# Kernel optimization log

Hardware: AMD Instinct MI355X
Metric: run time of the kernel (lower is better)

Reference implementation:

```python
import jax, jax.numpy as jnp
import numpy as np

PI = float(np.pi)


def _conv2d(x, w, b, pad):
    out = jax.lax.conv_general_dilated(x, w, (1, 1), ((pad, pad), (pad, pad)),
                                       dimension_numbers=('NCHW', 'OIHW', 'NCHW'))
    return out + b[None, :, None, None]


def _group_norm(x, gamma, beta, groups, eps=1e-5):
    B, C, h, w = x.shape
    xg = x.reshape(B, groups, C // groups, h, w)
    mu = xg.mean(axis=(2, 3, 4), keepdims=True)
    var = xg.var(axis=(2, 3, 4), keepdims=True)
    xn = ((xg - mu) / jnp.sqrt(var + eps)).reshape(B, C, h, w)
    return xn * gamma[None, :, None, None] + beta[None, :, None, None]


def _l2n(x, eps=1e-12):
    return x / jnp.maximum(jnp.linalg.norm(x, axis=1, keepdims=True), eps)


def _dense_sift(x):
    # kornia DenseSIFTDescriptor defaults: 8 ang bins, 4x4 spatial bins,
    # spatial_bin_size=4, rootsift=True, clipval=0.2, stride=1, padding=1
    eps = 1e-10
    NA = 8
    # 'diff' spatial gradient with replicate padding, normalized (/2)
    xp = jnp.pad(x, ((0, 0), (0, 0), (1, 1), (1, 1)), mode='edge')
    gx = (xp[:, :, 1:-1, 2:] - xp[:, :, 1:-1, :-2]) * 0.5
    gy = (xp[:, :, 2:, 1:-1] - xp[:, :, :-2, 1:-1]) * 0.5
    mag = jnp.sqrt(gx * gx + gy * gy + eps)[:, 0]           # [B,H,W]
    ori = jnp.arctan2(gy, gx + eps)[:, 0] + 2.0 * PI
    o_big = NA * ori / (2.0 * PI)
    bo0f = jnp.floor(o_big)
    wo1_ = o_big - bo0f
    wo0 = (1.0 - wo1_) * mag
    wo1 = wo1_ * mag
    bo0 = bo0f.astype(jnp.int32) % NA
    bo1 = (bo0 + 1) % NA
    bins = jnp.arange(NA).reshape(1, NA, 1, 1)
    ang = ((bo0[:, None] == bins).astype(x.dtype) * wo0[:, None]
           + (bo1[:, None] == bins).astype(x.dtype) * wo1[:, None])  # [B,8,H,W]
    # SIFT pooling kernel ksize=4 (triangle weights), conv pad=2 -> H+1,W+1
    xc2 = np.array([0.5, 1.5, 1.5, 0.5], np.float32)
    pool1 = np.outer(xc2, xc2) / 4.0
    pk = jnp.asarray(np.tile(pool1[None, None], (NA, 1, 1, 1)))  # depthwise [8,1,4,4]
    pooled = jax.lax.conv_general_dilated(ang, pk, (1, 1), ((2, 2), (2, 2)),
                dimension_numbers=('NCHW', 'OIHW', 'NCHW'), feature_group_count=NA)
    # identity reshape conv: 128 = 8 ang * 4*4 spatial bins, pad=1 -> back to H,W
    rk = jnp.asarray(np.eye(128, dtype=np.float32).reshape(128, NA, 4, 4))
    out = jax.lax.conv_general_dilated(pooled, rk, (1, 1), ((1, 1), (1, 1)),
                dimension_numbers=('NCHW', 'OIHW', 'NCHW'))
    out = jnp.clip(_l2n(out), 0.0, 0.2)
    out = _l2n(out)
    l1 = jnp.maximum(jnp.sum(jnp.abs(out), axis=1, keepdims=True), 1e-12)
    return jnp.sqrt(out / l1 + eps)  # rootsift


def _joint_bilateral(x, guide, ksize=5, sigma_color=0.1, sigma_space=1.5):
    pad = ksize // 2
    ax = np.arange(ksize, dtype=np.float32) - ksize // 2
    g1 = np.exp(-ax ** 2 / (2.0 * sigma_space ** 2))
    g1 = g1 / g1.sum()
    sk = np.outer(g1, g1)  # normalized 5x5 gaussian space kernel
    xp = jnp.pad(x, ((0, 0), (0, 0), (pad, pad), (pad, pad)), mode='reflect')
    gp = jnp.pad(guide, ((0, 0), (0, 0), (pad, pad), (pad, pad)), mode='reflect')
    h, w = x.shape[2], x.shape[3]
    inv = -0.5 / (sigma_color ** 2)
    num = jnp.zeros_like(x)
    den = jnp.zeros((x.shape[0], 1, h, w), x.dtype)
    for dy in range(ksize):           # fixed 5x5 tap loop, accumulated in-place
        for dx in range(ksize):
            gs = gp[:, :, dy:dy + h, dx:dx + w]
            cd = jnp.sum(jnp.abs(gs - guide), axis=1, keepdims=True) ** 2  # l1 squared
            wgt = sk[dy, dx] * jnp.exp(inv * cd)
            num = num + wgt * xp[:, :, dy:dy + h, dx:dx + w]
            den = den + wgt
    return num / den


def _forward(x, gt, w1, b1, g1w, g1b, w2, b2, g2w, g2b, w3, b3, g3w, g3b,
             w4, b4, g4w, g4b, w5, b5):
    orig = x
    f = _dense_sift(x)
    f = jax.nn.relu(_group_norm(_conv2d(f, w1, b1, 2), g1w, g1b, 8))
    f = jax.nn.relu(_group_norm(_conv2d(f, w2, b2, 1), g2w, g2b, 8))
    f = jax.nn.relu(_group_norm(_conv2d(f, w3, b3, 1), g3w, g3b, 4))
    f = jax.nn.relu(_group_norm(_conv2d(f, w4, b4, 1), g4w, g4b, 4))
    f = _conv2d(f, w5, b5, 1)
    # rgb_to_yuv(gt)[:, 1:] as guidance
    r, g, b = gt[:, 0], gt[:, 1], gt[:, 2]
    u = -0.147 * r - 0.289 * g + 0.436 * b
    v = 0.615 * r - 0.515 * g - 0.100 * b
    guide = jnp.stack([u, v], axis=1)
    f = _joint_bilateral(f, guide)

    def _rescale(c, lo, hi):
        c = (c - c.min()) / (c.max() - c.min() + 1e-6)  # global min/max over B,H,W
        c = jnp.clip(c, 0.0, 1.0)
        return c * (hi - lo) + lo

    U = _rescale(f[:, 0], -0.436, 0.436)
    V = _rescale(f[:, 1], -0.615, 0.615)
    Y = orig[:, 0]
    R = Y + 1.14 * V
    G = Y - 0.396 * U - 0.581 * V
    B = Y + 2.029 * U
    return jnp.stack([R, G, B], axis=1)


def setup_inputs() -> dict:
    key = jax.random.key(0)
    ks = jax.random.split(key, 16)
    B = 4
    d = {
        'x': jax.random.uniform(ks[0], (B, 1, 270, 512), jnp.float32),
        'gt': jax.random.uniform(ks[1], (B, 3, 270, 512), jnp.float32),
        'w1': jax.random.normal(ks[2], (64, 128, 5, 5), jnp.float32) * 0.02,
        'b1': jnp.zeros((64,), jnp.float32),
        'g1w': jnp.ones((64,), jnp.float32), 'g1b': jnp.zeros((64,), jnp.float32),
        'w2': jax.random.normal(ks[3], (32, 64, 3, 3), jnp.float32) * 0.04,
        'b2': jnp.zeros((32,), jnp.float32),
        'g2w': jnp.ones((32,), jnp.float32), 'g2b': jnp.zeros((32,), jnp.float32),
        'w3': jax.random.normal(ks[4], (16, 32, 3, 3), jnp.float32) * 0.05,
        'b3': jnp.zeros((16,), jnp.float32),
        'g3w': jnp.ones((16,), jnp.float32), 'g3b': jnp.zeros((16,), jnp.float32),
        'w4': jax.random.normal(ks[5], (8, 16, 3, 3), jnp.float32) * 0.08,
        'b4': jnp.zeros((8,), jnp.float32),
        'g4w': jnp.ones((8,), jnp.float32), 'g4b': jnp.zeros((8,), jnp.float32),
        'w5': jax.random.normal(ks[6], (2, 8, 3, 3), jnp.float32) * 0.1,
        'b5': jnp.zeros((2,), jnp.float32),
    }
    return d


def reference(x, gt, w1, b1, g1w, g1b, w2, b2, g2w, g2b, w3, b3, g3w, g3b,
              w4, b4, g4w, g4b, w5, b5):
    return _forward(x, gt, w1, b1, g1w, g1b, w2, b2, g2w, g2b, w3, b3, g3w, g3b,
                    w4, b4, g4w, g4b, w5, b5)
```

## Files before the change

kernel.cpp:

```cpp
#include <hip/hip_runtime.h>

constexpr int NB  = 4;
constexpr int IH  = 270;
constexpr int IW  = 512;
constexpr int NPIX = IH * IW;
constexpr int PH  = 271;
constexpr int PW  = 513;
constexpr float TWO_PI_F = 6.28318530717958647692f;

typedef short  bf16x8 __attribute__((ext_vector_type(8)));
typedef float floatx4 __attribute__((ext_vector_type(4)));

__device__ inline unsigned short f2bf(float x) {
  union { float f; unsigned u; } un; un.f = x;
  unsigned r = un.u + 0x7fff + ((un.u >> 16) & 1);
  return (unsigned short)(r >> 16);
}
__device__ inline float bf2f(unsigned short u) {
  union { unsigned u; float f; } x; x.u = ((unsigned)u) << 16; return x.f;
}
__device__ inline unsigned fkey(float f) {
  unsigned u = __float_as_uint(f);
  return (u & 0x80000000u) ? ~u : (u | 0x80000000u);
}
__device__ inline float funkey(unsigned k) {
  unsigned u = (k & 0x80000000u) ? (k ^ 0x80000000u) : ~k;
  return __uint_as_float(u);
}
__device__ inline void gn_coef_thread(const float* __restrict__ stats,
                                      const float* __restrict__ gamma,
                                      const float* __restrict__ beta,
                                      float* cA, float* cB, int C, int chper, int b) {
  int c = threadIdx.x;
  if (c < C) {
    int g0 = (c / chper) * chper;
    float S = 0.f, S2 = 0.f;
    for (int k = 0; k < chper; k++) {
      S  += stats[(b * C + g0 + k) * 2];
      S2 += stats[(b * C + g0 + k) * 2 + 1];
    }
    double Nd = (double)chper * NPIX;
    double mu = (double)S / Nd;
    double var = (double)S2 / Nd - mu * mu;
    double rstd = 1.0 / sqrt(var + 1e-5);
    float A = (float)rstd * gamma[c];
    cA[c] = A;
    cB[c] = beta[c] - (float)mu * A;
  }
}

__device__ inline void mfma_pack_one(const float* __restrict__ w, short* __restrict__ wB,
                                     int i, int CO, int CI, int KK, int CHUNKS) {
  int j = i & 7, l = (i >> 3) & 63, f = i >> 9;
  int t = f % KK; int fc = f / KK; int cc = fc % CHUNKS; int g = fc / CHUNKS;
  int ci = cc * 32 + ((l >> 4) << 3) + j;
  int co = g * 16 + (l & 15);
  float v = (ci < CI && co < CO) ? w[((size_t)co * CI + ci) * KK + t] : 0.f;
  wB[i] = (short)f2bf(v);
}
__device__ inline void repack_one(const float* __restrict__ w, float* __restrict__ wT,
                                  int i, int CO, int CI, int KK) {
  int o = i / (CI * KK);
  int r = i % (CI * KK);
  int ci = r / KK, kk = r % KK;
  wT[(kk * CI + ci) * CO + o] = w[i];
}
__global__ __launch_bounds__(256) void prep_kernel(
    const float* __restrict__ w1, const float* __restrict__ w2,
    const float* __restrict__ w3, const float* __restrict__ w4,
    const float* __restrict__ w5,
    short* __restrict__ w1B, short* __restrict__ w2B, short* __restrict__ w3B,
    float* __restrict__ w4T, float* __restrict__ w5T) {
  constexpr int N1 = 4 * 4 * 25 * 512;
  constexpr int N2 = 2 * 2 * 9 * 512;
  constexpr int N3 = 1 * 1 * 9 * 512;
  constexpr int N4 = 8 * 16 * 9;
  constexpr int N5 = 2 * 8 * 9;
  int i = blockIdx.x * 256 + threadIdx.x;
  if (i < N1) { mfma_pack_one(w1, w1B, i, 64, 128, 25, 4); return; }
  i -= N1;
  if (i < N2) { mfma_pack_one(w2, w2B, i, 32, 64, 9, 2); return; }
  i -= N2;
  if (i < N3) { mfma_pack_one(w3, w3B, i, 16, 32, 9, 1); return; }
  i -= N3;
  if (i < N4) { repack_one(w4, w4T, i, 8, 16, 9); return; }
  i -= N4;
  if (i < N5) { repack_one(w5, w5T, i, 2, 8, 9); return; }
}

__global__ __launch_bounds__(256) void sift_desc_kernel(
    const float* __restrict__ x, short* __restrict__ descg) {
  const int b = blockIdx.z;
  const int x0 = blockIdx.x * 16, y0 = blockIdx.y * 16;
  __shared__ float xs[24][25];
  __shared__ float wo0[22][23], wo1[22][23];
  __shared__ int   bo0[22][23];
  __shared__ float pooled[8][19][20];
  __shared__ float s1s[256], gs[256];
  const int tid = threadIdx.x;
  const float* xb = x + (size_t)b * NPIX;

  for (int t = tid; t < 576; t += 256) {
    int r = t / 24, c = t % 24;
    int gy = min(max(y0 - 4 + r, 0), IH - 1);
    int gx = min(max(x0 - 4 + c, 0), IW - 1);
    xs[r][c] = xb[gy * IW + gx];
  }
  __syncthreads();

  for (int t = tid; t < 484; t += 256) {
    int r = t / 22, c = t % 22;
    int gy = y0 - 3 + r, gx = x0 - 3 + c;
    float w0 = 0.f, w1v = 0.f; int b0 = 0;
    if (gy >= 0 && gy < IH && gx >= 0 && gx < IW) {
      float gxv = (xs[r + 1][c + 2] - xs[r + 1][c]) * 0.5f;
      float gyv = (xs[r + 2][c + 1] - xs[r][c + 1]) * 0.5f;
      float mag = sqrtf(gxv * gxv + gyv * gyv + 1e-10f);
      float ori = atan2f(gyv, gxv + 1e-10f) + TWO_PI_F;
      float obig = ori * (8.0f / TWO_PI_F);
      float bf = floorf(obig);
      float w1_ = obig - bf;
      w0  = (1.0f - w1_) * mag;
      w1v = w1_ * mag;
      b0  = ((int)bf) & 7;
    }
    wo0[r][c] = w0; wo1[r][c] = w1v; bo0[r][c] = b0;
  }
  __syncthreads();

  const float pwt[4] = {0.25f, 0.75f, 0.75f, 0.25f};
  for (int t = tid; t < 361; t += 256) {
    int pr = t / 19, pc = t % 19;
    int py = y0 - 1 + pr, px = x0 - 1 + pc;
    float acc[8] = {0, 0, 0, 0, 0, 0, 0, 0};
    if (py >= 0 && py < PH && px >= 0 && px < PW) {
      #pragma unroll
      for (int i = 0; i < 4; i++) {
        #pragma unroll
        for (int j = 0; j < 4; j++) {
          float w0 = wo0[pr + i][pc + j], w1v = wo1[pr + i][pc + j];
          int b0 = bo0[pr + i][pc + j];
          int b1i = (b0 + 1) & 7;
          float pw = pwt[i] * pwt[j];
          #pragma unroll
          for (int a = 0; a < 8; a++) {
            float add = (a == b0 ? w0 : 0.f) + (a == b1i ? w1v : 0.f);
            acc[a] = fmaf(pw, add, acc[a]);
          }
        }
      }
    }
    #pragma unroll
    for (int a = 0; a < 8; a++) pooled[a][pr][pc] = acc[a];
  }
  __syncthreads();

  {
    int py = tid >> 4, px = tid & 15;
    int y = y0 + py;
    float s1 = 0.f, g = 0.f;
    if (y < IH) {
      float sum2 = 0.f;
      for (int c = 0; c < 128; c++) {
        int a = c >> 4, i = (c >> 2) & 3, j = c & 3;
        float p = pooled[a][py + i][px + j];
        sum2 = fmaf(p, p, sum2);
      }
      s1 = 1.0f / fmaxf(sqrtf(sum2), 1e-12f);
      float st2 = 0.f, st = 0.f;
      for (int c = 0; c < 128; c++) {
        int a = c >> 4, i = (c >> 2) & 3, j = c & 3;
        float p = pooled[a][py + i][px + j];
        float tv = fminf(p * s1, 0.2f);
        st2 = fmaf(tv, tv, st2);
        st += tv;
      }
      float s2 = 1.0f / fmaxf(sqrtf(st2), 1e-12f);
      float l1 = fmaxf(s2 * st, 1e-12f);
      g = s2 / l1;
    }
    s1s[tid] = s1; gs[tid] = g;
  }
  __syncthreads();

  for (int k = 0; k < 16; k++) {
    int gidx = k * 256 + tid;
    int cc = gidx >> 10, pix = (gidx >> 2) & 255, sub = gidx & 3;
    int py = pix >> 4, px = pix & 15;
    int y = y0 + py;
    if (y >= IH) continue;
    float s1v = s1s[pix], gv = gs[pix];
    int a = cc * 2 + (sub >> 1);
    unsigned short v8[8];
    #pragma unroll
    for (int jj = 0; jj < 8; jj++) {
      int i = (sub * 2 + (jj >> 2)) & 3;
      int j = jj & 3;
      float p = pooled[a][py + i][px + j];
      v8[jj] = f2bf(sqrtf(fminf(p * s1v, 0.2f) * gv + 1e-10f));
    }
    uint4 pk;
    pk.x = (unsigned)v8[0] | ((unsigned)v8[1] << 16);
    pk.y = (unsigned)v8[2] | ((unsigned)v8[3] << 16);
    pk.z = (unsigned)v8[4] | ((unsigned)v8[5] << 16);
    pk.w = (unsigned)v8[6] | ((unsigned)v8[7] << 16);
    size_t base = ((size_t)(b * 4 + cc) * NPIX + (size_t)y * IW + (x0 + px)) * 32 + sub * 8;
    *(uint4*)(descg + base) = pk;
  }
}

__global__ __launch_bounds__(512, 2) void conv1_mfma_kernel(
    const short* __restrict__ descg, const short* __restrict__ w1B,
    const float* __restrict__ bias, unsigned short* __restrict__ out,
    float* __restrict__ stats) {
  const int b = blockIdx.z;
  const int x0 = blockIdx.x * 16, y0 = blockIdx.y * 16;
  __shared__ __align__(16) char smem_raw[33408];
  short* desc = (short*)smem_raw;
  float* cout = (float*)smem_raw;

  const int tid = threadIdx.x;
  const int wave = tid >> 6, lane = tid & 63;
  const int quad = lane >> 4, lm = lane & 15;
  const int nh = wave & 1, mh = wave >> 1;

  floatx4 acc[2][4];
  #pragma unroll
  for (int j = 0; j < 2; j++)
    #pragma unroll
    for (int i = 0; i < 4; i++) acc[j][i] = (floatx4){0.f, 0.f, 0.f, 0.f};

  for (int cc = 0; cc < 4; cc++) {
    __syncthreads();
    const short* dg = descg + (size_t)(b * 4 + cc) * NPIX * 32;
    for (int u = tid; u < 1600; u += 512) {
      int pos = u >> 2, sub = u & 3;
      int r = pos / 20, c = pos % 20;
      int gy = y0 - 2 + r, gx = x0 - 2 + c;
      uint4 val = {0u, 0u, 0u, 0u};
      if (gy >= 0 && gy < IH && gx >= 0 && gx < IW)
        val = *(const uint4*)(dg + ((size_t)gy * IW + gx) * 32 + sub * 8);
      *(uint4*)(desc + pos * 40 + sub * 8) = val;
    }
    __syncthreads();

    const short* wb = w1B + (size_t)cc * 25 * 512 + (lane << 3);
    bf16x8 bfrC[2], bfrN[2];
    #pragma unroll
    for (int j = 0; j < 2; j++)
      bfrN[j] = *(const bf16x8*)(wb + (size_t)(nh * 2 + j) * 100 * 512);
    #pragma unroll
    for (int t = 0; t < 25; t++) {
      int ky = t / 5, kx = t % 5;
      #pragma unroll
      for (int j = 0; j < 2; j++) bfrC[j] = bfrN[j];
      if (t < 24) {
        int t1 = t + 1;
        #pragma unroll
        for (int j = 0; j < 2; j++)
          bfrN[j] = *(const bf16x8*)(wb + ((size_t)(nh * 2 + j) * 100 + t1) * 512);
      }
      bf16x8 av[4];
      #pragma unroll
      for (int i = 0; i < 4; i++)
        av[i] = *(const bf16x8*)(desc + ((mh * 4 + i + ky) * 20 + lm + kx) * 40 + quad * 8);
      #pragma unroll
      for (int j = 0; j < 2; j++)
        #pragma unroll
        for (int i = 0; i < 4; i++)
          acc[j][i] = __builtin_amdgcn_mfma_f32_16x16x32_bf16(av[i], bfrC[j], acc[j][i], 0, 0, 0);
    }
  }

  unsigned short* ob = out + (size_t)b * 64 * NPIX;
  for (int h = 0; h < 2; h++) {
    __syncthreads();
    if (nh == h) {
      #pragma unroll
      for (int j = 0; j < 2; j++)
        #pragma unroll
        for (int i = 0; i < 4; i++)
          #pragma unroll
          for (int r = 0; r < 4; r++)
            cout[(j * 16 + lm) * 261 + (mh * 4 + i) * 16 + quad * 4 + r] = acc[j][i][r];
    }
    __syncthreads();
    for (int v = tid; v < 8192; v += 512) {
      int col = v >> 8, px = v & 255;
      int y = y0 + (px >> 4), x = x0 + (px & 15);
      if (y < IH)
        ob[(size_t)(h * 32 + col) * NPIX + y * IW + x] = f2bf(cout[col * 261 + px] + bias[h * 32 + col]);
    }
    int col = tid >> 4, seg = tid & 15;
    int co = h * 32 + col;
    float bv = bias[co];
    float sum = 0.f, sq = 0.f;
    if (y0 + seg < IH) {
      #pragma unroll
      for (int k = 0; k < 16; k++) {
        float vv = cout[col * 261 + seg * 16 + k] + bv;
        sum += vv; sq += vv * vv;
      }
    }
    sum += __shfl_down(sum, 8, 16); sq += __shfl_down(sq, 8, 16);
    sum += __shfl_down(sum, 4, 16); sq += __shfl_down(sq, 4, 16);
    sum += __shfl_down(sum, 2, 16); sq += __shfl_down(sq, 2, 16);
    sum += __shfl_down(sum, 1, 16); sq += __shfl_down(sq, 1, 16);
    if (seg == 0) {
      atomicAdd(&stats[(b * 64 + co) * 2], sum);
      atomicAdd(&stats[(b * 64 + co) * 2 + 1], sq);
    }
  }
}

template <int CI, int CO, int CHPER, bool STATS>
__global__ __launch_bounds__(256) void convk3_mfma_kernel(
    const unsigned short* __restrict__ xin, const short* __restrict__ wB,
    const float* __restrict__ bias, const float* __restrict__ statsIn,
    const float* __restrict__ gamma, const float* __restrict__ beta,
    float* __restrict__ statsOut, unsigned short* __restrict__ out) {
  constexpr int CHUNKS = CI / 32;
  constexpr int G = CO / 16;
  constexpr int MPW = 2 * G;
  constexpr int CIS = CI + 8;
  constexpr int TILE_B = 180 * CIS * 2;
  constexpr int COUT_B = CO * 133 * 4;
  constexpr int UNION_B = TILE_B > COUT_B ? TILE_B : COUT_B;
  __shared__ __align__(16) char sm[UNION_B + CI * 8];
  short* tile = (short*)sm;
  float* cout = (float*)sm;
  float* cA = (float*)(sm + UNION_B);
  float* cB = cA + CI;

  const int b = blockIdx.z;
  const int x0 = blockIdx.x * 16, y0 = blockIdx.y * 8;
  const int tid = threadIdx.x;
  const int wave = tid >> 6, lane = tid & 63;
  const int quad = lane >> 4, lm = lane & 15;
  const int n = wave % G, mh = wave / G;

  gn_coef_thread(statsIn, gamma, beta, cA, cB, CI, CHPER, b);
  __syncthreads();

  const unsigned short* xb = xin + (size_t)b * CI * NPIX;
  for (int v = tid; v < (CI / 2) * 180; v += 256) {
    int cp = v / 180, pos = v % 180;
    int r = pos / 18, c = pos % 18;
    int gy = y0 - 1 + r, gx = x0 - 1 + c;
    float v0 = 0.f, v1 = 0.f;
    if (gy >= 0 && gy < IH && gx >= 0 && gx < IW) {
      v0 = fmaxf(fmaf(bf2f(xb[(size_t)(2 * cp) * NPIX + gy * IW + gx]), cA[2 * cp], cB[2 * cp]), 0.f);
      v1 = fmaxf(fmaf(bf2f(xb[(size_t)(2 * cp + 1) * NPIX + gy * IW + gx]), cA[2 * cp + 1], cB[2 * cp + 1]), 0.f);
    }
    unsigned pk = (unsigned)f2bf(v0) | ((unsigned)f2bf(v1) << 16);
    *(unsigned*)(tile + pos * CIS + 2 * cp) = pk;
  }
  __syncthreads();

  floatx4 acc[MPW];
  #pragma unroll
  for (int i = 0; i < MPW; i++) acc[i] = (floatx4){0.f, 0.f, 0.f, 0.f};

  constexpr int NT = CHUNKS * 9;
  const short* wbase = wB + ((size_t)n * NT) * 512 + (lane << 3);
  bf16x8 bfrC, avC[MPW], bfrN, avN[MPW];
  bfrN = *(const bf16x8*)(wbase);
  #pragma unroll
  for (int i = 0; i < MPW; i++)
    avN[i] = *(const bf16x8*)(tile + ((mh * MPW + i) * 18 + lm) * CIS + quad * 8);
  #pragma unroll
  for (int t = 0; t < NT; t++) {
    bfrC = bfrN;
    #pragma unroll
    for (int i = 0; i < MPW; i++) avC[i] = avN[i];
    if (t < NT - 1) {
      int t1 = t + 1;
      int cc1 = t1 / 9, r1 = t1 % 9, ky1 = r1 / 3, kx1 = r1 % 3;
      bfrN = *(const bf16x8*)(wbase + (size_t)t1 * 512);
      #pragma unroll
      for (int i = 0; i < MPW; i++)
        avN[i] = *(const bf16x8*)(tile + ((mh * MPW + i + ky1) * 18 + lm + kx1) * CIS + cc1 * 32 + quad * 8);
    }
    #pragma unroll
    for (int i = 0; i < MPW; i++)
      acc[i] = __builtin_amdgcn_mfma_f32_16x16x32_bf16(avC[i], bfrC, acc[i], 0, 0, 0);
  }
  __syncthreads();
  #pragma unroll
  for (int i = 0; i < MPW; i++) {
    #pragma unroll
    for (int r = 0; r < 4; r++) {
      int pixel = (mh * MPW + i) * 16 + quad * 4 + r;
      cout[(n * 16 + lm) * 133 + pixel] = acc[i][r];
    }
  }
  __syncthreads();
  unsigned short* ob = out + (size_t)b * CO * NPIX;
  for (int v = tid; v < CO * 128; v += 256) {
    int co = v >> 7, px = v & 127;
    int y = y0 + (px >> 4), x = x0 + (px & 15);
    if (y < IH) ob[(size_t)co * NPIX + y * IW + x] = f2bf(cout[co * 133 + px] + bias[co]);
  }
  if (STATS) {
    constexpr int TPC = 256 / CO;
    constexpr int PXT = 128 / TPC;
    int col = tid / TPC, seg = tid % TPC;
    float bv = bias[col];
    float sum = 0.f, sq = 0.f;
    #pragma unroll
    for (int k = 0; k < PXT; k++) {
      int p = seg * PXT + k;
      if (y0 + (p >> 4) < IH) {
        float vv = cout[col * 133 + p] + bv;
        sum += vv; sq += vv * vv;
      }
    }
    #pragma unroll
    for (int off = TPC / 2; off > 0; off >>= 1) {
      sum += __shfl_down(sum, off);
      sq  += __shfl_down(sq, off);
    }
    if (seg == 0) {
      atomicAdd(&statsOut[(b * CO + col) * 2], sum);
      atomicAdd(&statsOut[(b * CO + col) * 2 + 1], sq);
    }
  }
}

template <int CI, int CO, int CHPER, bool STATS, bool OUT_BF16>
__global__ __launch_bounds__(256) void convs_kernel(
    const unsigned short* __restrict__ xin, const float* __restrict__ wT,
    const float* __restrict__ bias, const float* __restrict__ statsIn,
    const float* __restrict__ gamma, const float* __restrict__ beta,
    float* __restrict__ statsOut, void* __restrict__ outv) {
  constexpr int OPT = CO / 2;
  const int b = blockIdx.z;
  const int x0 = blockIdx.x * 16, y0 = blockIdx.y * 8;
  __shared__ float tile[CI * 180];
  __shared__ float cA[CI], cB[CI];
  __shared__ float ssum[CO], ssq[CO];
  gn_coef_thread(statsIn, gamma, beta, cA, cB, CI, CHPER, b);
  if (STATS && threadIdx.x < CO) { ssum[threadIdx.x] = 0.f; ssq[threadIdx.x] = 0.f; }
  __syncthreads();
  const unsigned short* xb = xin + (size_t)b * CI * NPIX;
  for (int t = threadIdx.x; t < CI * 180; t += 256) {
    int ci = t / 180, rc = t % 180, r = rc / 18, c = rc % 18;
    int gy = y0 - 1 + r, gx = x0 - 1 + c;
    float v = 0.f;
    if (gy >= 0 && gy < IH && gx >= 0 && gx < IW)
      v = fmaxf(fmaf(bf2f(xb[(size_t)ci * NPIX + gy * IW + gx]), cA[ci], cB[ci]), 0.f);
    tile[t] = v;
  }
  __syncthreads();
  const int t = threadIdx.x;
  const int px = t & 127, og = t >> 7;
  const int pyy = px >> 4, pxx = px & 15;
  const int oc0 = og * OPT;
  const int y = y0 + pyy, x = x0 + pxx;
  float acc[OPT] = {};
  for (int ky = 0; ky < 3; ky++) {
    for (int kx = 0; kx < 3; kx++) {
      const float* wrow = wT + (size_t)((ky * 3 + kx) * CI) * CO + oc0;
      for (int ci = 0; ci < CI; ci++) {
        float v = tile[ci * 180 + (pyy + ky) * 18 + pxx + kx];
        #pragma unroll
        for (int o = 0; o < OPT; o++) acc[o] = fmaf(v, wrow[ci * CO + o], acc[o]);
      }
    }
  }
  if (y < IH) {
    #pragma unroll
    for (int o = 0; o < OPT; o++) {
      float vv = acc[o] + bias[oc0 + o];
      if (OUT_BF16) {
        unsigned short* ob = (unsigned short*)outv + (size_t)b * CO * NPIX;
        ob[(size_t)(oc0 + o) * NPIX + y * IW + x] = f2bf(vv);
      } else {
        float* ob = (float*)outv + (size_t)b * CO * NPIX;
        ob[(size_t)(oc0 + o) * NPIX + y * IW + x] = vv;
      }
      if (STATS) {
        atomicAdd(&ssum[oc0 + o], vv);
        atomicAdd(&ssq[oc0 + o], vv * vv);
      }
    }
  }
  if (STATS) {
    __syncthreads();
    if (threadIdx.x < CO) {
      atomicAdd(&statsOut[(b * CO + threadIdx.x) * 2], ssum[threadIdx.x]);
      atomicAdd(&statsOut[(b * CO + threadIdx.x) * 2 + 1], ssq[threadIdx.x]);
    }
  }
}

__global__ __launch_bounds__(256) void bilateral_kernel(
    const float* __restrict__ f, const float* __restrict__ gt,
    float* __restrict__ out, unsigned* __restrict__ mmbits) {
  const int b = blockIdx.z;
  const int x0 = blockIdx.x * 16, y0 = blockIdx.y * 16;
  __shared__ float gu[20][20], gv[20][20], f0s[20][20], f1s[20][20];
  __shared__ float red[4][4];
  const float* gtb = gt + (size_t)b * 3 * NPIX;
  const float* fb = f + (size_t)b * 2 * NPIX;
  for (int t = threadIdx.x; t < 400; t += 256) {
    int r = t / 20, c = t % 20;
    int gy = y0 - 2 + r, gx = x0 - 2 + c;
    if (gy < 0) gy = -gy;
    if (gy > IH - 1) gy = 2 * (IH - 1) - gy;
    if (gx < 0) gx = -gx;
    if (gx > IW - 1) gx = 2 * (IW - 1) - gx;
    int p = gy * IW + gx;
    float rr = gtb[p], gg = gtb[NPIX + p], bb = gtb[2 * NPIX + p];
    gu[r][c]  = -0.147f * rr - 0.289f * gg + 0.436f * bb;
    gv[r][c]  =  0.615f * rr - 0.515f * gg - 0.100f * bb;
    f0s[r][c] = fb[p];
    f1s[r][c] = fb[NPIX + p];
  }
  __syncthreads();
  const int t = threadIdx.x;
  const int lx = t % 16, ly = t / 16;
  const int y = y0 + ly, x = x0 + lx;
  const bool valid = (y < IH);

  float o0 = 0.f, o1 = 0.f;
  if (valid) {
    float g1v[5];
    float s = 0.f;
    #pragma unroll
    for (int k = 0; k < 5; k++) {
      float a = (float)(k - 2);
      g1v[k] = expf(-a * a / 4.5f);
      s += g1v[k];
    }
    #pragma unroll
    for (int k = 0; k < 5; k++) g1v[k] /= s;
    float cu = gu[ly + 2][lx + 2], cv = gv[ly + 2][lx + 2];
    float num0 = 0.f, num1 = 0.f, den = 0.f;
    #pragma unroll
    for (int dy = 0; dy < 5; dy++) {
      #pragma unroll
      for (int dx = 0; dx < 5; dx++) {
        float du = fabsf(gu[ly + dy][lx + dx] - cu) + fabsf(gv[ly + dy][lx + dx] - cv);
        float wgt = g1v[dy] * g1v[dx] * expf(-50.0f * du * du);
        num0 = fmaf(wgt, f0s[ly + dy][lx + dx], num0);
        num1 = fmaf(wgt, f1s[ly + dy][lx + dx], num1);
        den += wgt;
      }
    }
    o0 = num0 / den; o1 = num1 / den;
    float* ob = out + (size_t)b * 2 * NPIX;
    ob[y * IW + x] = o0;
    ob[NPIX + y * IW + x] = o1;
  }
  float mn0 = valid ? o0 : 1e30f,  mx0 = valid ? o0 : -1e30f;
  float mn1 = valid ? o1 : 1e30f,  mx1 = valid ? o1 : -1e30f;
  #pragma unroll
  for (int off = 32; off > 0; off >>= 1) {
    mn0 = fminf(mn0, __shfl_xor(mn0, off));
    mx0 = fmaxf(mx0, __shfl_xor(mx0, off));
    mn1 = fminf(mn1, __shfl_xor(mn1, off));
    mx1 = fmaxf(mx1, __shfl_xor(mx1, off));
  }
  if ((t & 63) == 0) {
    red[t >> 6][0] = mn0; red[t >> 6][1] = mx0;
    red[t >> 6][2] = mn1; red[t >> 6][3] = mx1;
  }
  __syncthreads();
  if (t == 0) {
    for (int w = 1; w < 4; w++) {
      red[0][0] = fminf(red[0][0], red[w][0]);
      red[0][1] = fmaxf(red[0][1], red[w][1]);
      red[0][2] = fminf(red[0][2], red[w][2]);
      red[0][3] = fmaxf(red[0][3], red[w][3]);
    }
    atomicMax(&mmbits[0], fkey(red[0][1]));
    atomicMax(&mmbits[1], fkey(red[0][3]));
    atomicMin(&mmbits[2], fkey(red[0][0]));
    atomicMin(&mmbits[3], fkey(red[0][2]));
  }
}

__global__ __launch_bounds__(256) void final_kernel(
    const float* __restrict__ bil, const float* __restrict__ x,
    const unsigned* __restrict__ mmbits, float* __restrict__ out) {
  int i = blockIdx.x * 256 + threadIdx.x;
  if (i >= NB * NPIX) return;
  float mx0 = funkey(mmbits[0]), mx1 = funkey(mmbits[1]);
  float mn0 = funkey(mmbits[2]), mn1 = funkey(mmbits[3]);
  int b = i / NPIX, p = i % NPIX;
  float f0 = bil[(size_t)b * 2 * NPIX + p];
  float f1 = bil[(size_t)b * 2 * NPIX + NPIX + p];
  float U = (f0 - mn0) / (mx0 - mn0 + 1e-6f);
  U = fminf(fmaxf(U, 0.f), 1.f) * 0.872f - 0.436f;
  float V = (f1 - mn1) / (mx1 - mn1 + 1e-6f);
  V = fminf(fmaxf(V, 0.f), 1.f) * 1.23f - 0.615f;
  float Y = x[(size_t)b * NPIX + p];
  float* ob = out + (size_t)b * 3 * NPIX;
  ob[p]            = Y + 1.14f * V;
  ob[NPIX + p]     = Y - 0.396f * U - 0.581f * V;
  ob[2 * NPIX + p] = Y + 2.029f * U;
}

extern "C" void kernel_launch(void* const* d_in, const int* in_sizes, int n_in,
                              void* d_out, int out_size, void* d_ws, size_t ws_size,
                              hipStream_t stream) {
  const float* x   = (const float*)d_in[0];
  const float* gt  = (const float*)d_in[1];
  const float* w1  = (const float*)d_in[2];
  const float* b1  = (const float*)d_in[3];
  const float* g1w = (const float*)d_in[4];
  const float* g1b = (const float*)d_in[5];
  const float* w2  = (const float*)d_in[6];
  const float* b2  = (const float*)d_in[7];
  const float* g2w = (const float*)d_in[8];
  const float* g2b = (const float*)d_in[9];
  const float* w3  = (const float*)d_in[10];
  const float* b3  = (const float*)d_in[11];
  const float* g3w = (const float*)d_in[12];
  const float* g3b = (const float*)d_in[13];
  const float* w4  = (const float*)d_in[14];
  const float* b4  = (const float*)d_in[15];
  const float* g4w = (const float*)d_in[16];
  const float* g4b = (const float*)d_in[17];
  const float* w5  = (const float*)d_in[18];
  const float* b5  = (const float*)d_in[19];
  float* out = (float*)d_out;

  char* ws = (char*)d_ws;
  float* stats1 = (float*)ws;
  float* stats2 = stats1 + 512;
  float* stats3 = stats2 + 256;
  float* stats4 = stats3 + 128;
  unsigned* mmbits = (unsigned*)(ws + 12288);
  char* base = ws + 16384;
  short* descg = (short*)base;
  size_t descg_shorts = (size_t)NB * 4 * NPIX * 32;
  unsigned short* bufB_h = (unsigned short*)base;
  float* c5    = (float*)(base + 36000000);
  float* bilat = (float*)(base + 41000000);
  short* w1B = descg + descg_shorts;
  short* w2B = w1B + 204800;
  short* w3B = w2B + 18432;
  float* w4T = (float*)(w3B + 4608);
  float* w5T = w4T + 1152;
  unsigned short* bufA_h = (unsigned short*)(w5T + 144);

  hipMemsetAsync(ws, 0, 12304, stream);
  hipMemsetAsync(ws + 12296, 0xFF, 8, stream);

  prep_kernel<<<896, 256, 0, stream>>>(w1, w2, w3, w4, w5, w1B, w2B, w3B, w4T, w5T);

  sift_desc_kernel<<<dim3(32, 17, NB), 256, 0, stream>>>(x, descg);

  conv1_mfma_kernel<<<dim3(32, 17, NB), 512, 0, stream>>>(descg, w1B, b1, bufA_h, stats1);

  convk3_mfma_kernel<64, 32, 8, true><<<dim3(32, 34, NB), 256, 0, stream>>>(
      bufA_h, w2B, b2, stats1, g1w, g1b, stats2, bufB_h);

  convk3_mfma_kernel<32, 16, 4, true><<<dim3(32, 34, NB), 256, 0, stream>>>(
      bufB_h, w3B, b3, stats2, g2w, g2b, stats3, bufA_h);

  convs_kernel<16, 8, 4, true, true><<<dim3(32, 34, NB), 256, 0, stream>>>(
      bufA_h, w4T, b4, stats3, g3w, g3b, stats4, bufB_h);

  convs_kernel<8, 2, 2, false, false><<<dim3(32, 34, NB), 256, 0, stream>>>(
      bufB_h, w5T, b5, stats4, g4w, g4b, nullptr, c5);

  bilateral_kernel<<<dim3(32, 17, NB), 256, 0, stream>>>(c5, gt, bilat, mmbits);
  final_kernel<<<(NB * NPIX + 255) / 256, 256, 0, stream>>>(bilat, x, mmbits, out);

  (void)in_sizes; (void)n_in; (void)out_size; (void)ws_size;
}
```

Baseline: 1.300 ms.

## Shrink conv1 tiles to 8x8 with 4 waves and reshape weight prefetch

Conv1 now uses 8x8 output tiles with 256-thread blocks, and each wave owns 16 output channels across all 64 pixels. The previous layout used 16x16 tiles, 512 threads and a 2x4 wave split. The smaller tile cuts shared memory and registers, which allows more blocks to be resident. In exchange the halo overhead rises sharply (12x12 loaded per 8x8 versus 20x20 per 16x16), and each block now re-reads the full 64-channel weight set. Weight prefetch becomes a two-slot ring in both conv1 and the 3x3 MFMA kernel. The 3x3 kernel also stops prefetching activation fragments from LDS one step ahead.

```diff
diff --git a/kernel.cpp b/kernel.cpp
--- a/kernel.cpp
+++ b/kernel.cpp
@@ -209,33 +209,30 @@
   }
 }
 
-__global__ __launch_bounds__(512, 2) void conv1_mfma_kernel(
+__global__ __launch_bounds__(256) void conv1_mfma_kernel(
     const short* __restrict__ descg, const short* __restrict__ w1B,
     const float* __restrict__ bias, unsigned short* __restrict__ out,
     float* __restrict__ stats) {
   const int b = blockIdx.z;
-  const int x0 = blockIdx.x * 16, y0 = blockIdx.y * 16;
-  __shared__ __align__(16) char smem_raw[33408];
+  const int x0 = blockIdx.x * 8, y0 = blockIdx.y * 8;
+  __shared__ __align__(16) char smem_raw[16640];
   short* desc = (short*)smem_raw;
   float* cout = (float*)smem_raw;
 
   const int tid = threadIdx.x;
   const int wave = tid >> 6, lane = tid & 63;
   const int quad = lane >> 4, lm = lane & 15;
-  const int nh = wave & 1, mh = wave >> 1;
-
-  floatx4 acc[2][4];
+
+  floatx4 acc[4];
   #pragma unroll
-  for (int j = 0; j < 2; j++)
-    #pragma unroll
-    for (int i = 0; i < 4; i++) acc[j][i] = (floatx4){0.f, 0.f, 0.f, 0.f};
+  for (int i = 0; i < 4; i++) acc[i] = (floatx4){0.f, 0.f, 0.f, 0.f};
 
   for (int cc = 0; cc < 4; cc++) {
     __syncthreads();
     const short* dg = descg + (size_t)(b * 4 + cc) * NPIX * 32;
-    for (int u = tid; u < 1600; u += 512) {
+    for (int u = tid; u < 576; u += 256) {
       int pos = u >> 2, sub = u & 3;
-      int r = pos / 20, c = pos % 20;
+      int r = pos / 12, c = pos % 12;
       int gy = y0 - 2 + r, gx = x0 - 2 + c;
       uint4 val = {0u, 0u, 0u, 0u};
       if (gy >= 0 && gy < IH && gx >= 0 && gx < IW)
@@ -244,71 +241,55 @@
     }
     __syncthreads();
 
-    const short* wb = w1B + (size_t)cc * 25 * 512 + (lane << 3);
-    bf16x8 bfrC[2], bfrN[2];
-    #pragma unroll
-    for (int j = 0; j < 2; j++)
-      bfrN[j] = *(const bf16x8*)(wb + (size_t)(nh * 2 + j) * 100 * 512);
+    const short* wb = w1B + ((size_t)(wave * 4 + cc) * 25) * 512 + (lane << 3);
+    bf16x8 bfr[2];
+    bfr[0] = *(const bf16x8*)(wb);
+    bfr[1] = *(const bf16x8*)(wb + 512);
     #pragma unroll
     for (int t = 0; t < 25; t++) {
-      int ky = t / 5, kx = t % 5;
+      const int ky = t / 5, kx = t % 5, sl = t & 1;
+      bf16x8 bcur = bfr[sl];
+      if (t + 2 < 25) bfr[sl] = *(const bf16x8*)(wb + (size_t)(t + 2) * 512);
       #pragma unroll
-      for (int j = 0; j < 2; j++) bfrC[j] = bfrN[j];
-      if (t < 24) {
-        int t1 = t + 1;
-        #pragma unroll
-        for (int j = 0; j < 2; j++)
-          bfrN[j] = *(const bf16x8*)(wb + ((size_t)(nh * 2 + j) * 100 + t1) * 512);
-      }
-      bf16x8 av[4];
-      #pragma unroll
-      for (int i = 0; i < 4; i++)
-        av[i] = *(const bf16x8*)(desc + ((mh * 4 + i + ky) * 20 + lm + kx) * 40 + quad * 8);
-      #pragma unroll
-      for (int j = 0; j < 2; j++)
-        #pragma unroll
-        for (int i = 0; i < 4; i++)
-          acc[j][i] = __builtin_amdgcn_mfma_f32_16x16x32_bf16(av[i], bfrC[j], acc[j][i], 0, 0, 0);
-    }
-  }
-
+      for (int i = 0; i < 4; i++) {
+        int pixel = i * 16 + lm;
+        int py = pixel >> 3, px = pixel & 7;
+        bf16x8 av = *(const bf16x8*)(desc + ((py + ky) * 12 + px + kx) * 40 + quad * 8);
+        acc[i] = __builtin_amdgcn_mfma_f32_16x16x32_bf16(av, bcur, acc[i], 0, 0, 0);
+      }
+    }
+  }
+
+  __syncthreads();
+  #pragma unroll
+  for (int i = 0; i < 4; i++)
+    #pragma unroll
+    for (int r = 0; r < 4; r++)
+      cout[(wave * 16 + lm) * 65 + i * 16 + quad * 4 + r] = acc[i][r];
+  __syncthreads();
   unsigned short* ob = out + (size_t)b * 64 * NPIX;
-  for (int h = 0; h < 2; h++) {
-    __syncthreads();
-    if (nh == h) {
-      #pragma unroll
-      for (int j = 0; j < 2; j++)
-        #pragma unroll
-        for (int i = 0; i < 4; i++)
-          #pragma unroll
-          for (int r = 0; r < 4; r++)
-            cout[(j * 16 + lm) * 261 + (mh * 4 + i) * 16 + quad * 4 + r] = acc[j][i][r];
-    }
-    __syncthreads();
-    for (int v = tid; v < 8192; v += 512) {
-      int col = v >> 8, px = v & 255;
-      int y = y0 + (px >> 4), x = x0 + (px & 15);
-      if (y < IH)
-        ob[(size_t)(h * 32 + col) * NPIX + y * IW + x] = f2bf(cout[col * 261 + px] + bias[h * 32 + col]);
-    }
-    int col = tid >> 4, seg = tid & 15;
-    int co = h * 32 + col;
-    float bv = bias[co];
+  for (int v = tid; v < 4096; v += 256) {
+    int co = v >> 6, px = v & 63;
+    int y = y0 + (px >> 3), x = x0 + (px & 7);
+    if (y < IH) ob[(size_t)co * NPIX + y * IW + x] = f2bf(cout[co * 65 + px] + bias[co]);
+  }
+  {
+    int col = tid >> 2, seg = tid & 3;
+    float bv = bias[col];
     float sum = 0.f, sq = 0.f;
-    if (y0 + seg < IH) {
-      #pragma unroll
-      for (int k = 0; k < 16; k++) {
-        float vv = cout[col * 261 + seg * 16 + k] + bv;
+    #pragma unroll
+    for (int k = 0; k < 16; k++) {
+      int p = seg * 16 + k;
+      if (y0 + (p >> 3) < IH) {
+        float vv = cout[col * 65 + p] + bv;
         sum += vv; sq += vv * vv;
       }
     }
-    sum += __shfl_down(sum, 8, 16); sq += __shfl_down(sq, 8, 16);
-    sum += __shfl_down(sum, 4, 16); sq += __shfl_down(sq, 4, 16);
-    sum += __shfl_down(sum, 2, 16); sq += __shfl_down(sq, 2, 16);
-    sum += __shfl_down(sum, 1, 16); sq += __shfl_down(sq, 1, 16);
+    sum += __shfl_down(sum, 2, 4); sq += __shfl_down(sq, 2, 4);
+    sum += __shfl_down(sum, 1, 4); sq += __shfl_down(sq, 1, 4);
     if (seg == 0) {
-      atomicAdd(&stats[(b * 64 + co) * 2], sum);
-      atomicAdd(&stats[(b * 64 + co) * 2 + 1], sq);
+      atomicAdd(&stats[(b * 64 + col) * 2], sum);
+      atomicAdd(&stats[(b * 64 + col) * 2 + 1], sq);
     }
   }
 }
@@ -363,27 +344,22 @@
 
   constexpr int NT = CHUNKS * 9;
   const short* wbase = wB + ((size_t)n * NT) * 512 + (lane << 3);
-  bf16x8 bfrC, avC[MPW], bfrN, avN[MPW];
-  bfrN = *(const bf16x8*)(wbase);
-  #pragma unroll
-  for (int i = 0; i < MPW; i++)
-    avN[i] = *(const bf16x8*)(tile + ((mh * MPW + i) * 18 + lm) * CIS + quad * 8);
+  bf16x8 bfr[2];
+  bfr[0] = *(const bf16x8*)(wbase);
+  bfr[1] = *(const bf16x8*)(wbase + 512);
   #pragma unroll
   for (int t = 0; t < NT; t++) {
-    bfrC = bfrN;
-    #pragma unroll
-    for (int i = 0; i < MPW; i++) avC[i] = avN[i];
-    if (t < NT - 1) {
-      int t1 = t + 1;
-      int cc1 = t1 / 9, r1 = t1 % 9, ky1 = r1 / 3, kx1 = r1 % 3;
-      bfrN = *(const bf16x8*)(wbase + (size_t)t1 * 512);
-      #pragma unroll
-      for (int i = 0; i < MPW; i++)
-        avN[i] = *(const bf16x8*)(tile + ((mh * MPW + i + ky1) * 18 + lm + kx1) * CIS + cc1 * 32 + quad * 8);
-    }
+    const int sl = t & 1;
+    const int cc1 = t / 9, r1 = t % 9, ky = r1 / 3, kx = r1 % 3;
+    bf16x8 av[MPW];
     #pragma unroll
     for (int i = 0; i < MPW; i++)
-      acc[i] = __builtin_amdgcn_mfma_f32_16x16x32_bf16(avC[i], bfrC, acc[i], 0, 0, 0);
+      av[i] = *(const bf16x8*)(tile + ((mh * MPW + i + ky) * 18 + lm + kx) * CIS + cc1 * 32 + quad * 8);
+    #pragma unroll
+    for (int i = 0; i < MPW; i++)
+      acc[i] = __builtin_amdgcn_mfma_f32_16x16x32_bf16(av[i], bfr[sl], acc[i], 0, 0, 0);
+    if (t + 2 < NT)
+      bfr[sl] = *(const bf16x8*)(wbase + (size_t)(t + 2) * 512);
   }
   __syncthreads();
   #pragma unroll
@@ -653,7 +629,7 @@
 
   sift_desc_kernel<<<dim3(32, 17, NB), 256, 0, stream>>>(x, descg);
 
-  conv1_mfma_kernel<<<dim3(32, 17, NB), 512, 0, stream>>>(descg, w1B, b1, bufA_h, stats1);
+  conv1_mfma_kernel<<<dim3(64, 34, NB), 256, 0, stream>>>(descg, w1B, b1, bufA_h, stats1);
 
   convk3_mfma_kernel<64, 32, 8, true><<<dim3(32, 34, NB), 256, 0, stream>>>(
       bufA_h, w2B, b2, stats1, g1w, g1b, stats2, bufB_h);
```

New measurement: 1.342 ms. 3.2% more time.
